# Optimization experiments

Hardware: AMD Instinct MI355X
Metric: run time of the kernel (lower is better)

## Reference

```python
import jax, jax.numpy as jnp
import numpy as np

EPS_MSG = 1e-7
BN_EPS = 1e-5
LN_EPS = 1e-5


def setup_inputs() -> dict:
    key = jax.random.key(0)
    ks = jax.random.split(key, 8)
    N, E, D, H = 50000, 800000, 128, 256
    x = jax.random.normal(ks[0], (N, D), dtype=jnp.float32)
    edge_attr = jax.random.normal(ks[1], (E, 2), dtype=jnp.float32)
    edge_index = jax.random.randint(ks[2], (2, E), 0, N)
    edge_w = jax.random.normal(ks[3], (2, D), dtype=jnp.float32) * (1.0 / np.sqrt(2))
    edge_b = jnp.zeros((D,), jnp.float32)
    t = jnp.ones((1,), jnp.float32)
    w1 = jax.random.normal(ks[4], (D, H), dtype=jnp.float32) * (1.0 / np.sqrt(D))
    b1 = jnp.zeros((H,), jnp.float32)
    bn_gamma = jnp.ones((H,), jnp.float32)
    bn_beta = jnp.zeros((H,), jnp.float32)
    w2 = jax.random.normal(ks[5], (H, D), dtype=jnp.float32) * (1.0 / np.sqrt(H))
    b2 = jnp.zeros((D,), jnp.float32)
    ln_gamma = jnp.ones((D,), jnp.float32)
    ln_beta = jnp.zeros((D,), jnp.float32)
    return {"x": x, "edge_attr": edge_attr, "edge_w": edge_w, "edge_b": edge_b,
            "t": t, "w1": w1, "b1": b1, "bn_gamma": bn_gamma, "bn_beta": bn_beta,
            "w2": w2, "b2": b2, "ln_gamma": ln_gamma, "ln_beta": ln_beta,
            "edge_index": edge_index}


def reference(x, edge_attr, edge_w, edge_b, t, w1, b1, bn_gamma, bn_beta,
              w2, b2, ln_gamma, ln_beta, edge_index):
    N = x.shape[0]
    src, dst = edge_index[0], edge_index[1]
    # GENConv message: relu(x_j + edge_encoder(edge_attr)) + eps
    e = edge_attr @ edge_w + edge_b              # [E, D]
    msg = jax.nn.relu(x[src] + e) + EPS_MSG      # [E, D]
    # softmax aggregation per destination node, temperature t (per-feature)
    s = msg * t                                  # [E, D]
    mx = jax.ops.segment_max(s, dst, num_segments=N)
    mx = jnp.where(jnp.isfinite(mx), mx, 0.0)
    ex = jnp.exp(s - mx[dst])
    den = jax.ops.segment_sum(ex, dst, num_segments=N)
    alpha = ex / jnp.maximum(den[dst], 1e-16)
    agg = jax.ops.segment_sum(alpha * msg, dst, num_segments=N)  # [N, D]
    # root residual then update MLP: Linear -> BatchNorm -> ReLU -> Linear
    h = agg + x
    h1 = h @ w1 + b1                             # [N, 2D]
    mu = h1.mean(0)
    var = h1.var(0)
    h1 = (h1 - mu) / jnp.sqrt(var + BN_EPS) * bn_gamma + bn_beta
    h1 = jax.nn.relu(h1)
    out = h1 @ w2 + b2                           # [N, D]
    # LayerNorm + ELU (dropout = identity in eval)
    mu2 = out.mean(-1, keepdims=True)
    var2 = out.var(-1, keepdims=True)
    out = (out - mu2) / jnp.sqrt(var2 + LN_EPS) * ln_gamma + ln_beta
    return jax.nn.elu(out)
```

## Files before the change

### kernel.cpp

```cpp
#include <hip/hip_runtime.h>
#include <stdint.h>

typedef short bf16x8 __attribute__((ext_vector_type(8)));
typedef float f32x4  __attribute__((ext_vector_type(4)));
typedef float f32x2  __attribute__((ext_vector_type(2)));

#define BCAP 2032

__device__ __forceinline__ uint16_t fbu(float f){
    union { float f; uint32_t i; } v; v.f = f;
    uint32_t r = v.i + 0x7FFFu + ((v.i >> 16) & 1u);
    return (uint16_t)(r >> 16);
}
__device__ __forceinline__ float bfu(uint16_t u){
    union { uint32_t i; float f; } v; v.i = ((uint32_t)u) << 16; return v.f;
}
__device__ __forceinline__ uint32_t pk2(float v0, float v1){
    return __builtin_amdgcn_perm(__float_as_uint(v1), __float_as_uint(v0), 0x07060302u);
}
__device__ __forceinline__ float fexp2(float x){
#if __has_builtin(__builtin_amdgcn_exp2f)
    return __builtin_amdgcn_exp2f(x);
#else
    float r; asm("v_exp_f32 %0, %1" : "=v"(r) : "v"(x)); return r;
#endif
}

__global__ __launch_bounds__(256) void k_front(
    const float* __restrict__ x, uint16_t* __restrict__ xb, int n4, int nbx,
    const float* __restrict__ w1, const float* __restrict__ w2,
    uint16_t* __restrict__ w1t, uint16_t* __restrict__ w2t)
{
    int b = blockIdx.x, tid = threadIdx.x;
    if (b < nbx){
        int i = b*256 + tid;
        if (i < n4){
            float4 v = *(const float4*)(x + (size_t)i*4);
            ushort4 o;
            o.x = fbu(v.x); o.y = fbu(v.y); o.z = fbu(v.z); o.w = fbu(v.w);
            *(ushort4*)(xb + (size_t)i*4) = o;
        }
    } else {
        int idx = (b - nbx)*256 + tid;
        if (idx < 128*256){
            int k = idx >> 8, n = idx & 255;
            w1t[n*128 + k] = fbu(w1[idx]);
        } else {
            int j = idx - 128*256;
            int k = j >> 7, n = j & 127;
            w2t[n*256 + k] = fbu(w2[j]);
        }
    }
}

__global__ __launch_bounds__(1024) void k_bin(
    const int* __restrict__ src, const int* __restrict__ dst,
    const float* __restrict__ eattr,
    int* __restrict__ gcnt, uint2* __restrict__ breg, int E, int nbkt)
{
    __shared__ uint2 spay[8192];
    __shared__ int cnt[1024];
    __shared__ int base[1024];
    __shared__ int gbase[1024];
    __shared__ int wsum[16];
    int tid = threadIdx.x;
    int lane = tid & 63, w = tid >> 6;
    int e0 = blockIdx.x * 8192;
    int nE = E - e0; if (nE > 8192) nE = 8192;

    for (int i = tid; i < 1024; i += 1024) cnt[i] = 0;
    __syncthreads();
    int d[8];
    #pragma unroll
    for (int j = 0; j < 8; ++j){
        int i = tid + j*1024;
        d[j] = (i < nE) ? dst[e0 + i] : -1;
        if (i < nE) atomicAdd(&cnt[d[j] >> 6], 1);
    }
    __syncthreads();
    int v = cnt[tid];
    int sv = v;
    #pragma unroll
    for (int o = 1; o < 64; o <<= 1){ int t2 = __shfl_up(sv, o); if (lane >= o) sv += t2; }
    if (lane == 63) wsum[w] = sv;
    __syncthreads();
    if (tid < 16){
        int ws_ = wsum[tid];
        #pragma unroll
        for (int o = 1; o < 16; o <<= 1){ int t2 = __shfl_up(ws_, o); if (tid >= o) ws_ += t2; }
        wsum[tid] = ws_;
    }
    __syncthreads();
    int excl = (sv - v) + ((w == 0) ? 0 : wsum[w-1]);
    base[tid] = excl;
    if (tid < nbkt && v > 0) gbase[tid] = atomicAdd(&gcnt[tid], v);
    cnt[tid] = excl;
    __syncthreads();
    #pragma unroll
    for (int j = 0; j < 8; ++j){
        int i = tid + j*1024;
        if (i < nE){
            int e = e0 + i;
            int s = src[e];
            float2 a = *(const float2*)(eattr + (size_t)e*2);
            int bkt = d[j] >> 6;
            int pos = atomicAdd(&cnt[bkt], 1);
            uint2 p;
            p.x = (uint32_t)s | ((uint32_t)d[j] << 16);
            p.y = (uint32_t)fbu(a.x) | ((uint32_t)fbu(a.y) << 16);
            spay[pos] = p;
        }
    }
    __syncthreads();
    for (int i = tid; i < nE; i += 1024){
        uint2 p = spay[i];
        int bkt = (int)(p.x >> 22);
        int g = gbase[bkt] + (i - base[bkt]);
        breg[(size_t)bkt * BCAP + g] = p;
    }
}

__global__ __launch_bounds__(1024) void k_bscan(const int* __restrict__ gcnt,
                                                int* __restrict__ bbase, int nbkt){
    __shared__ int wsum[16];
    int tid = threadIdx.x;
    int lane = tid & 63, w = tid >> 6;
    int v = (tid < nbkt) ? gcnt[tid] : 0;
    int sv = v;
    #pragma unroll
    for (int o = 1; o < 64; o <<= 1){ int t2 = __shfl_up(sv, o); if (lane >= o) sv += t2; }
    if (lane == 63) wsum[w] = sv;
    __syncthreads();
    if (tid < 16){
        int ws_ = wsum[tid];
        #pragma unroll
        for (int o = 1; o < 16; o <<= 1){ int t2 = __shfl_up(ws_, o); if (tid >= o) ws_ += t2; }
        wsum[tid] = ws_;
    }
    __syncthreads();
    if (tid < nbkt) bbase[tid] = (sv - v) + ((w == 0) ? 0 : wsum[w-1]);
}

__global__ __launch_bounds__(256) void k_bsort(
    const uint2* __restrict__ breg, const int* __restrict__ gcnt,
    const int* __restrict__ bbase, uint2* __restrict__ se,
    int* __restrict__ offs, int Nn)
{
    __shared__ uint2 pay[BCAP];
    __shared__ uint2 pay2[BCAP];
    __shared__ int ncnt[64];
    int b = blockIdx.x;
    int tid = threadIdx.x;
    int cnt = gcnt[b];
    int base = bbase[b];
    if (b == 0 && tid == 0) offs[0] = 0;
    if (tid < 64) ncnt[tid] = 0;
    __syncthreads();
    for (int i = tid; i < cnt; i += 256){
        uint2 p = breg[(size_t)b * BCAP + i];
        pay[i] = p;
        atomicAdd(&ncnt[(p.x >> 16) & 63], 1);
    }
    __syncthreads();
    if (tid < 64){
        int v = ncnt[tid];
        int sv = v;
        #pragma unroll
        for (int o = 1; o < 64; o <<= 1){ int t2 = __shfl_up(sv, o); if (tid >= o) sv += t2; }
        int node = b*64 + tid;
        if (node < Nn) offs[node + 1] = base + sv;
        ncnt[tid] = sv - v;
    }
    __syncthreads();
    for (int i = tid; i < cnt; i += 256){
        uint2 p = pay[i];
        int pos = atomicAdd(&ncnt[(p.x >> 16) & 63], 1);
        pay2[pos] = make_uint2(p.x & 0xFFFFu, p.y);
    }
    __syncthreads();
    for (int i = tid; i < cnt; i += 256)
        se[base + i] = pay2[i];
}

__global__ __launch_bounds__(256) void k_agg(
    const uint16_t* __restrict__ xb, const uint2* __restrict__ se,
    const float* __restrict__ ew, const float* __restrict__ ebias,
    const float* __restrict__ tptr, const int* __restrict__ offs,
    uint16_t* __restrict__ h, int Nn)
{
    int lane = threadIdx.x & 63;
    int n = blockIdx.x * 4 + (threadIdx.x >> 6);
    if (n >= Nn) return;
    int d0 = lane * 2;
    float tt2 = tptr[0] * 1.44269504f;
    f32x2 wa0 = { ew[d0]*tt2,     ew[d0+1]*tt2 };
    f32x2 wa1 = { ew[128+d0]*tt2, ew[128+d0+1]*tt2 };
    f32x2 bbt = { ebias[d0]*tt2,  ebias[d0+1]*tt2 };
    const f32x2 zero2 = { 0.f, 0.f };
    int beg = offs[n], end = offs[n+1];
    f32x2 den = zero2, num = zero2;
    int i0 = beg;
    for (; i0 + 16 <= end; i0 += 16){
        uint2 md = se[i0 + (lane & 15)];
        int mxs = (int)md.x;
        int mys = (int)md.y;
        uint32_t xw[16];
        #pragma unroll
        for (int j = 0; j < 16; ++j){
            uint32_t sj = (uint32_t)__builtin_amdgcn_readlane(mxs, j) & 0xFFFFu;
            xw[j] = *(const uint32_t*)(xb + ((size_t)sj << 7) + d0);
        }
        #pragma unroll
        for (int j = 0; j < 16; ++j){
            uint32_t aw = (uint32_t)__builtin_amdgcn_readlane(mys, j);
            float a0 = bfu((uint16_t)aw), a1 = bfu((uint16_t)(aw >> 16));
            uint32_t u = xw[j];
            f32x2 xv = { bfu((uint16_t)u), bfu((uint16_t)(u >> 16)) };
            f32x2 p = xv * tt2 + (wa0 * a0 + wa1 * a1 + bbt);
            p = __builtin_elementwise_max(p, zero2);
            f32x2 ex = { fexp2(p.x), fexp2(p.y) };
            den += ex;
            num += ex * p;
        }
    }
    int rem = end - i0;
    if (rem > 0){
        uint2 md = make_uint2(0u, 0u);
        if ((lane & 15) < rem) md = se[i0 + (lane & 15)];
        int mxs = (int)md.x;
        int mys = (int)md.y;
        uint32_t xw[16];
        #pragma unroll
        for (int j = 0; j < 16; ++j){
            uint32_t sj = (uint32_t)__builtin_amdgcn_readlane(mxs, j) & 0xFFFFu;
            if (j < rem) xw[j] = *(const uint32_t*)(xb + ((size_t)sj << 7) + d0);
        }
        #pragma unroll
        for (int j = 0; j < 16; ++j){
            if (j < rem){
                uint32_t aw = (uint32_t)__builtin_amdgcn_readlane(mys, j);
                float a0 = bfu((uint16_t)aw), a1 = bfu((uint16_t)(aw >> 16));
                uint32_t u = xw[j];
                f32x2 xv = { bfu((uint16_t)u), bfu((uint16_t)(u >> 16)) };
                f32x2 p = xv * tt2 + (wa0 * a0 + wa1 * a1 + bbt);
                p = __builtin_elementwise_max(p, zero2);
                f32x2 ex = { fexp2(p.x), fexp2(p.y) };
                den += ex;
                num += ex * p;
            }
        }
    }
    float agg0 = num.x / fmaxf(den.x * tt2, 1e-16f) + 1e-7f;
    float agg1 = num.y / fmaxf(den.y * tt2, 1e-16f) + 1e-7f;
    uint32_t xr = *(const uint32_t*)(xb + (size_t)n*128 + d0);
    float v0 = agg0 + bfu((uint16_t)xr);
    float v1 = agg1 + bfu((uint16_t)(xr >> 16));
    *(uint32_t*)(h + (size_t)n*128 + d0) = pk2(v0, v1);
}

__global__ __launch_bounds__(256) void k_gemm1(
    const uint16_t* __restrict__ h, const uint16_t* __restrict__ w1t,
    const float* __restrict__ b1, float* __restrict__ bnsum, float* __restrict__ bnss,
    uint16_t* __restrict__ h1, int M)
{
    __shared__ uint16_t tile[64*264];
    int lane = threadIdx.x & 63;
    int wid  = threadIdx.x >> 6;
    int row0 = blockIdx.x * 64;
    int cb   = wid * 64;
    int lr   = lane & 15;
    int lk   = (lane >> 4) * 8;
    f32x4 acc[4][4] = {};
    #pragma unroll
    for (int ks = 0; ks < 4; ++ks){
        int k = ks*32 + lk;
        bf16x8 a[4], b[4];
        #pragma unroll
        for (int rt = 0; rt < 4; ++rt){
            int r = row0 + rt*16 + lr; if (r > M-1) r = M-1;
            a[rt] = *(const bf16x8*)(h + (size_t)r*128 + k);
        }
        #pragma unroll
        for (int ct = 0; ct < 4; ++ct){
            int c = cb + ct*16 + lr;
            b[ct] = *(const bf16x8*)(w1t + (size_t)c*128 + k);
        }
        #pragma unroll
        for (int rt = 0; rt < 4; ++rt)
            #pragma unroll
            for (int ct = 0; ct < 4; ++ct)
                acc[rt][ct] = __builtin_amdgcn_mfma_f32_16x16x32_bf16(a[rt], b[ct], acc[rt][ct], 0, 0, 0);
    }
    int co = (lane >> 4) * 4;
    #pragma unroll
    for (int ct = 0; ct < 4; ++ct){
        int c = cb + ct*16 + lr;
        float bias = b1[c];
        float ps = 0.f, ps2 = 0.f;
        #pragma unroll
        for (int rt = 0; rt < 4; ++rt){
            #pragma unroll
            for (int rg = 0; rg < 4; ++rg){
                int rl = rt*16 + co + rg;
                float v = acc[rt][ct][rg] + bias;
                tile[rl*264 + c] = fbu(v);
                if (row0 + rl < M){ ps += v; ps2 += v*v; }
            }
        }
        ps  += __shfl_xor(ps, 16);  ps  += __shfl_xor(ps, 32);
        ps2 += __shfl_xor(ps2, 16); ps2 += __shfl_xor(ps2, 32);
        if ((lane >> 4) == 0){
            atomicAdd(&bnsum[c], ps);
            atomicAdd(&bnss[c], ps2);
        }
    }
    __syncthreads();
    #pragma unroll
    for (int j = 0; j < 8; ++j){
        int idx8  = j*256 + threadIdx.x;
        int rr    = idx8 & 15;
        int kc    = (idx8 >> 4) & 31;
        int rt16l = idx8 >> 9;
        if (row0 + rt16l*16 + rr < M){
            bf16x8 v = *(const bf16x8*)(tile + (rt16l*16 + rr)*264 + kc*8);
            *(bf16x8*)(h1 + (size_t)row0*256 + (size_t)idx8*8) = v;
        }
    }
}

__global__ __launch_bounds__(256) void k_gemm2(
    const uint16_t* __restrict__ h1, const uint16_t* __restrict__ w2t,
    const float* __restrict__ bnsum, const float* __restrict__ bnss,
    const float* __restrict__ bng, const float* __restrict__ bnb,
    const float* __restrict__ b2, const float* __restrict__ lng,
    const float* __restrict__ lnb, float* __restrict__ out, int M, float invM)
{
    __shared__ float sbn_s[256], tbn_s[256];
    __shared__ float2 red[64][2];
    int tid = threadIdx.x;
    {
        float mu  = bnsum[tid] * invM;
        float var = bnss[tid] * invM - mu*mu;
        float rstd = rsqrtf(fmaxf(var, 0.f) + 1e-5f);
        float sc = rstd * bng[tid];
        sbn_s[tid] = sc;
        tbn_s[tid] = bnb[tid] - mu * sc;
    }
    __syncthreads();
    int lane = tid & 63;
    int wid  = tid >> 6;
    int wm = wid >> 1, wn = wid & 1;
    int row0 = blockIdx.x * 64;
    int lr = lane & 15, lkg = lane >> 4;
    int rt16max = (M - 1) >> 4;
    f32x4 acc[2][4] = {};
    #pragma unroll
    for (int ks = 0; ks < 8; ++ks){
        int k = ks*32 + lkg*8;
        float s[8], t[8];
        *(float4*)&s[0] = *(const float4*)(sbn_s + k);
        *(float4*)&s[4] = *(const float4*)(sbn_s + k + 4);
        *(float4*)&t[0] = *(const float4*)(tbn_s + k);
        *(float4*)&t[4] = *(const float4*)(tbn_s + k + 4);
        bf16x8 a[2], b[4];
        #pragma unroll
        for (int rt = 0; rt < 2; ++rt){
            int rt16 = (row0 >> 4) + wm*2 + rt;
            if (rt16 > rt16max) rt16 = rt16max;
            bf16x8 hv = *(const bf16x8*)(h1 + (size_t)rt16*4096 + (size_t)(ks*4 + lkg)*128 + lr*8);
            union { uint32_t u[4]; bf16x8 v; } pk;
            #pragma unroll
            for (int jj = 0; jj < 4; ++jj){
                float v0 = fmaf(bfu((uint16_t)hv[2*jj]),   s[2*jj],   t[2*jj]);
                float v1 = fmaf(bfu((uint16_t)hv[2*jj+1]), s[2*jj+1], t[2*jj+1]);
                v0 = fmaxf(v0, 0.f); v1 = fmaxf(v1, 0.f);
                pk.u[jj] = pk2(v0, v1);
            }
            a[rt] = pk.v;
        }
        #pragma unroll
        for (int ct = 0; ct < 4; ++ct){
            int c = wn*64 + ct*16 + lr;
            b[ct] = *(const bf16x8*)(w2t + (size_t)c*256 + k);
        }
        #pragma unroll
        for (int rt = 0; rt < 2; ++rt)
            #pragma unroll
            for (int ct = 0; ct < 4; ++ct)
                acc[rt][ct] = __builtin_amdgcn_mfma_f32_16x16x32_bf16(a[rt], b[ct], acc[rt][ct], 0, 0, 0);
    }
    float lngv[4], lnbv[4];
    #pragma unroll
    for (int ct = 0; ct < 4; ++ct){
        int cl = wn*64 + ct*16 + lr;
        float bias = b2[cl];
        lngv[ct] = lng[cl];
        lnbv[ct] = lnb[cl];
        #pragma unroll
        for (int rt = 0; rt < 2; ++rt)
            #pragma unroll
            for (int rg = 0; rg < 4; ++rg)
                acc[rt][ct][rg] += bias;
    }
    #pragma unroll
    for (int rt = 0; rt < 2; ++rt){
        #pragma unroll
        for (int rg = 0; rg < 4; ++rg){
            float s = 0.f, s2 = 0.f;
            #pragma unroll
            for (int ct = 0; ct < 4; ++ct){
                float v = acc[rt][ct][rg];
                s += v; s2 = fmaf(v, v, s2);
            }
            s  += __shfl_xor(s, 1);  s  += __shfl_xor(s, 2);  s  += __shfl_xor(s, 4);  s  += __shfl_xor(s, 8);
            s2 += __shfl_xor(s2, 1); s2 += __shfl_xor(s2, 2); s2 += __shfl_xor(s2, 4); s2 += __shfl_xor(s2, 8);
            if (lr == 0){
                int rl = wm*32 + rt*16 + lkg*4 + rg;
                red[rl][wn] = make_float2(s, s2);
            }
        }
    }
    __syncthreads();
    #pragma unroll
    for (int rt = 0; rt < 2; ++rt){
        #pragma unroll
        for (int rg = 0; rg < 4; ++rg){
            int rl = wm*32 + rt*16 + lkg*4 + rg;
            int gr = row0 + rl;
            float2 p0 = red[rl][0], p1 = red[rl][1];
            float sum  = p0.x + p1.x;
            float sum2 = p0.y + p1.y;
            float mu = sum * (1.f/128.f);
            float var = sum2 * (1.f/128.f) - mu*mu;
            float rstd = rsqrtf(fmaxf(var, 0.f) + 1e-5f);
            if (gr < M){
                #pragma unroll
                for (int ct = 0; ct < 4; ++ct){
                    int cl = wn*64 + ct*16 + lr;
                    float v = (acc[rt][ct][rg] - mu) * rstd * lngv[ct] + lnbv[ct];
                    v = (v > 0.f) ? v : (fexp2(v * 1.44269504f) - 1.f);
                    out[(size_t)gr*128 + cl] = v;
                }
            }
        }
    }
}

extern "C" void kernel_launch(void* const* d_in, const int* in_sizes, int n_in,
                              void* d_out, int out_size, void* d_ws, size_t ws_size,
                              hipStream_t stream)
{
    (void)n_in; (void)out_size; (void)ws_size;
    const float* x     = (const float*)d_in[0];
    const float* eattr = (const float*)d_in[1];
    const float* ew    = (const float*)d_in[2];
    const float* eb    = (const float*)d_in[3];
    const float* t     = (const float*)d_in[4];
    const float* w1    = (const float*)d_in[5];
    const float* b1    = (const float*)d_in[6];
    const float* bng   = (const float*)d_in[7];
    const float* bnb   = (const float*)d_in[8];
    const float* w2    = (const float*)d_in[9];
    const float* b2    = (const float*)d_in[10];
    const float* lng   = (const float*)d_in[11];
    const float* lnb   = (const float*)d_in[12];
    const int*   eidx  = (const int*)d_in[13];
    int Nn = in_sizes[0] / 128;
    int E  = in_sizes[13] / 2;
    int nbkt = (Nn + 63) >> 6;

    char* ws = (char*)d_ws;
    size_t off = 0;
    auto alloc = [&](size_t bytes)->char*{
        char* p = ws + off;
        off += (bytes + 511) & ~(size_t)511;
        return p;
    };
    char* zstart   = ws;
    int*   gcnt    = (int*)  alloc((size_t)nbkt * 4);
    float* bnsum   = (float*)alloc(256 * 4);
    float* bnss    = (float*)alloc(256 * 4);
    size_t zlen    = off;
    int*   bbase   = (int*)  alloc((size_t)nbkt * 4);
    int*   offs    = (int*)  alloc((size_t)(Nn + 1) * 4);
    uint2* se      = (uint2*)alloc((size_t)E * 8);
    uint16_t* w1t  = (uint16_t*)alloc(128 * 256 * 2);
    uint16_t* w2t  = (uint16_t*)alloc(128 * 256 * 2);
    uint16_t* hbuf = (uint16_t*)alloc((size_t)Nn * 128 * 2);

    uint16_t* xb   = (uint16_t*)d_out;
    uint2*    breg = (uint2*)((char*)d_out + (size_t)Nn * 128 * 2);
    uint16_t* h1   = (uint16_t*)d_out;
    float*    fo   = (float*)d_out;

    int n4  = Nn * 32;
    int nbx = (n4 + 255) / 256;
    int nbp = (2*128*256 + 255) / 256;

    hipMemsetAsync(zstart, 0, zlen, stream);
    k_front<<<nbx + nbp, 256, 0, stream>>>(x, xb, n4, nbx, w1, w2, w1t, w2t);
    k_bin<<<(E + 8191) / 8192, 1024, 0, stream>>>(eidx, eidx + E, eattr, gcnt, breg, E, nbkt);
    k_bscan<<<1, 1024, 0, stream>>>(gcnt, bbase, nbkt);
    k_bsort<<<nbkt, 256, 0, stream>>>(breg, gcnt, bbase, se, offs, Nn);
    k_agg<<<(Nn + 3) / 4, 256, 0, stream>>>(xb, se, ew, eb, t, offs, hbuf, Nn);
    k_gemm1<<<(Nn + 63) / 64, 256, 0, stream>>>(hbuf, w1t, b1, bnsum, bnss, h1, Nn);
    k_gemm2<<<(Nn + 63) / 64, 256, 0, stream>>>(h1, w2t, bnsum, bnss, bng, bnb, b2, lng, lnb, fo, Nn, 1.0f/(float)Nn);
}
```

Before: 139.3 us.

## Merge conversion kernel into edge binning launch and pre-tile weights for MFMA loads

The standalone x/weight bf16 conversion kernel is folded into the edge-binning kernel as extra 1024-thread blocks, removing one launch and letting conversion overlap with binning. Weights are now written in a fragment-major layout so each GEMM lane group reads 128 contiguous elements, giving coalesced B-operand loads in both GEMMs. The cost is that conversion blocks now run at the binning kernel's 1024-thread size and carry its large shared-memory allocation, which may limit occupancy for those blocks.

```diff
diff --git a/kernel.cpp b/kernel.cpp
--- a/kernel.cpp
+++ b/kernel.cpp
@@ -26,46 +26,47 @@
 #endif
 }
 
-__global__ __launch_bounds__(256) void k_front(
-    const float* __restrict__ x, uint16_t* __restrict__ xb, int n4, int nbx,
-    const float* __restrict__ w1, const float* __restrict__ w2,
-    uint16_t* __restrict__ w1t, uint16_t* __restrict__ w2t)
-{
-    int b = blockIdx.x, tid = threadIdx.x;
-    if (b < nbx){
-        int i = b*256 + tid;
-        if (i < n4){
-            float4 v = *(const float4*)(x + (size_t)i*4);
-            ushort4 o;
-            o.x = fbu(v.x); o.y = fbu(v.y); o.z = fbu(v.z); o.w = fbu(v.w);
-            *(ushort4*)(xb + (size_t)i*4) = o;
-        }
-    } else {
-        int idx = (b - nbx)*256 + tid;
-        if (idx < 128*256){
-            int k = idx >> 8, n = idx & 255;
-            w1t[n*128 + k] = fbu(w1[idx]);
-        } else {
-            int j = idx - 128*256;
-            int k = j >> 7, n = j & 127;
-            w2t[n*256 + k] = fbu(w2[j]);
-        }
-    }
-}
-
-__global__ __launch_bounds__(1024) void k_bin(
+__global__ __launch_bounds__(1024) void k_pre(
     const int* __restrict__ src, const int* __restrict__ dst,
     const float* __restrict__ eattr,
-    int* __restrict__ gcnt, uint2* __restrict__ breg, int E, int nbkt)
+    int* __restrict__ gcnt, uint2* __restrict__ breg, int E, int nbkt, int nb_bin,
+    const float* __restrict__ x, uint16_t* __restrict__ xb, int n4, int nb_x,
+    const float* __restrict__ w1, const float* __restrict__ w2,
+    uint16_t* __restrict__ w1g, uint16_t* __restrict__ w2g)
 {
     __shared__ uint2 spay[8192];
     __shared__ int cnt[1024];
     __shared__ int base[1024];
     __shared__ int gbase[1024];
     __shared__ int wsum[16];
-    int tid = threadIdx.x;
+    int b = blockIdx.x, tid = threadIdx.x;
+
+    if (b >= nb_bin){
+        int bb = b - nb_bin;
+        if (bb < nb_x){
+            int i = bb*1024 + tid;
+            if (i < n4){
+                float4 v = *(const float4*)(x + (size_t)i*4);
+                ushort4 o;
+                o.x = fbu(v.x); o.y = fbu(v.y); o.z = fbu(v.z); o.w = fbu(v.w);
+                *(ushort4*)(xb + (size_t)i*4) = o;
+            }
+        } else {
+            int j = (bb - nb_x)*1024 + tid;
+            if (j < 32768){
+                int e = j & 7, lr = (j >> 3) & 15, kc = (j >> 7) & 15, c16 = (j >> 11) & 15;
+                w1g[j] = fbu(w1[(size_t)(kc*8 + e)*256 + c16*16 + lr]);
+            } else {
+                int j2 = j - 32768;
+                int e = j2 & 7, lr = (j2 >> 3) & 15, kc = (j2 >> 7) & 31, c16 = (j2 >> 12) & 7;
+                w2g[j2] = fbu(w2[(size_t)(kc*8 + e)*128 + c16*16 + lr]);
+            }
+        }
+        return;
+    }
+
     int lane = tid & 63, w = tid >> 6;
-    int e0 = blockIdx.x * 8192;
+    int e0 = b * 8192;
     int nE = E - e0; if (nE > 8192) nE = 8192;
 
     for (int i = tid; i < 1024; i += 1024) cnt[i] = 0;
@@ -259,7 +260,7 @@
 }
 
 __global__ __launch_bounds__(256) void k_gemm1(
-    const uint16_t* __restrict__ h, const uint16_t* __restrict__ w1t,
+    const uint16_t* __restrict__ h, const uint16_t* __restrict__ w1g,
     const float* __restrict__ b1, float* __restrict__ bnsum, float* __restrict__ bnss,
     uint16_t* __restrict__ h1, int M)
 {
@@ -269,7 +270,8 @@
     int row0 = blockIdx.x * 64;
     int cb   = wid * 64;
     int lr   = lane & 15;
-    int lk   = (lane >> 4) * 8;
+    int lkg  = lane >> 4;
+    int lk   = lkg * 8;
     f32x4 acc[4][4] = {};
     #pragma unroll
     for (int ks = 0; ks < 4; ++ks){
@@ -282,8 +284,8 @@
         }
         #pragma unroll
         for (int ct = 0; ct < 4; ++ct){
-            int c = cb + ct*16 + lr;
-            b[ct] = *(const bf16x8*)(w1t + (size_t)c*128 + k);
+            int c16 = wid*4 + ct;
+            b[ct] = *(const bf16x8*)(w1g + ((size_t)(c16*16 + ks*4 + lkg) << 7) + lr*8);
         }
         #pragma unroll
         for (int rt = 0; rt < 4; ++rt)
@@ -291,7 +293,7 @@
             for (int ct = 0; ct < 4; ++ct)
                 acc[rt][ct] = __builtin_amdgcn_mfma_f32_16x16x32_bf16(a[rt], b[ct], acc[rt][ct], 0, 0, 0);
     }
-    int co = (lane >> 4) * 4;
+    int co = lkg * 4;
     #pragma unroll
     for (int ct = 0; ct < 4; ++ct){
         int c = cb + ct*16 + lr;
@@ -309,7 +311,7 @@
         }
         ps  += __shfl_xor(ps, 16);  ps  += __shfl_xor(ps, 32);
         ps2 += __shfl_xor(ps2, 16); ps2 += __shfl_xor(ps2, 32);
-        if ((lane >> 4) == 0){
+        if (lkg == 0){
             atomicAdd(&bnsum[c], ps);
             atomicAdd(&bnss[c], ps2);
         }
@@ -329,7 +331,7 @@
 }
 
 __global__ __launch_bounds__(256) void k_gemm2(
-    const uint16_t* __restrict__ h1, const uint16_t* __restrict__ w2t,
+    const uint16_t* __restrict__ h1, const uint16_t* __restrict__ w2g,
     const float* __restrict__ bnsum, const float* __restrict__ bnss,
     const float* __restrict__ bng, const float* __restrict__ bnb,
     const float* __restrict__ b2, const float* __restrict__ lng,
@@ -380,8 +382,8 @@
         }
         #pragma unroll
         for (int ct = 0; ct < 4; ++ct){
-            int c = wn*64 + ct*16 + lr;
-            b[ct] = *(const bf16x8*)(w2t + (size_t)c*256 + k);
+            int c16 = wn*4 + ct;
+            b[ct] = *(const bf16x8*)(w2g + ((size_t)(c16*32 + ks*4 + lkg) << 7) + lr*8);
         }
         #pragma unroll
         for (int rt = 0; rt < 2; ++rt)
@@ -484,8 +486,8 @@
     int*   bbase   = (int*)  alloc((size_t)nbkt * 4);
     int*   offs    = (int*)  alloc((size_t)(Nn + 1) * 4);
     uint2* se      = (uint2*)alloc((size_t)E * 8);
-    uint16_t* w1t  = (uint16_t*)alloc(128 * 256 * 2);
-    uint16_t* w2t  = (uint16_t*)alloc(128 * 256 * 2);
+    uint16_t* w1g  = (uint16_t*)alloc(128 * 256 * 2);
+    uint16_t* w2g  = (uint16_t*)alloc(128 * 256 * 2);
     uint16_t* hbuf = (uint16_t*)alloc((size_t)Nn * 128 * 2);
 
     uint16_t* xb   = (uint16_t*)d_out;
@@ -493,16 +495,18 @@
     uint16_t* h1   = (uint16_t*)d_out;
     float*    fo   = (float*)d_out;
 
-    int n4  = Nn * 32;
-    int nbx = (n4 + 255) / 256;
-    int nbp = (2*128*256 + 255) / 256;
+    int n4     = Nn * 32;
+    int nb_bin = (E + 8191) / 8192;
+    int nb_x   = (n4 + 1023) / 1024;
+    int nb_w   = (2*128*256 + 1023) / 1024;
 
     hipMemsetAsync(zstart, 0, zlen, stream);
-    k_front<<<nbx + nbp, 256, 0, stream>>>(x, xb, n4, nbx, w1, w2, w1t, w2t);
-    k_bin<<<(E + 8191) / 8192, 1024, 0, stream>>>(eidx, eidx + E, eattr, gcnt, breg, E, nbkt);
+    k_pre<<<nb_bin + nb_x + nb_w, 1024, 0, stream>>>(
+        eidx, eidx + E, eattr, gcnt, breg, E, nbkt, nb_bin,
+        x, xb, n4, nb_x, w1, w2, w1g, w2g);
     k_bscan<<<1, 1024, 0, stream>>>(gcnt, bbase, nbkt);
     k_bsort<<<nbkt, 256, 0, stream>>>(breg, gcnt, bbase, se, offs, Nn);
     k_agg<<<(Nn + 3) / 4, 256, 0, stream>>>(xb, se, ew, eb, t, offs, hbuf, Nn);
-    k_gemm1<<<(Nn + 63) / 64, 256, 0, stream>>>(hbuf, w1t, b1, bnsum, bnss, h1, Nn);
-    k_gemm2<<<(Nn + 63) / 64, 256, 0, stream>>>(h1, w2t, bnsum, bnss, bng, bnb, b2, lng, lnb, fo, Nn, 1.0f/(float)Nn);
-}
+    k_gemm1<<<(Nn + 63) / 64, 256, 0, stream>>>(hbuf, w1g, b1, bnsum, bnss, h1, Nn);
+    k_gemm2<<<(Nn + 63) / 64, 256, 0, stream>>>(h1, w2g, bnsum, bnss, bng, bnb, b2, lng, lnb, fo, Nn, 1.0f/(float)Nn);
+}
```

Measured after the change: 122.0 us, median of 2. -12.5%, faster.
